# Optimization experiments

Hardware: AMD Instinct MI355X
Metric: run time of the kernel (lower is better)

## Reference

```python
import jax, jax.numpy as jnp
import numpy as np

N, E = 20000, 320000
H = 4            # heads per layer
C_IN, C_HID, C_OUT = 128, 64, 64
NEG_SLOPE = 0.2  # PyG GATConv default leaky_relu slope


def setup_inputs() -> dict:
    key = jax.random.key(0)
    ks = jax.random.split(key, 16)
    p = lambda k, shape: jax.random.normal(k, shape, jnp.float32) * 0.1
    return {
        "x": jax.random.normal(ks[0], (N, C_IN), jnp.float32),
        "edge_index": jax.random.randint(ks[1], (2, E), 0, N),
        # layer 0: in C_IN -> H*C_HID (concat)
        "W0": p(ks[2], (C_IN, H * C_HID)),
        "as0": p(ks[3], (H, C_HID)),
        "ad0": p(ks[4], (H, C_HID)),
        "b0": jnp.zeros((H * C_HID,), jnp.float32),
        # layer 1: in H*C_HID -> H*C_HID (concat)
        "W1": p(ks[5], (H * C_HID, H * C_HID)),
        "as1": p(ks[6], (H, C_HID)),
        "ad1": p(ks[7], (H, C_HID)),
        "b1": jnp.zeros((H * C_HID,), jnp.float32),
        # output layer: in H*C_HID -> C_OUT (mean over heads, concat=False)
        "W2": p(ks[8], (H * C_HID, H * C_OUT)),
        "as2": p(ks[9], (H, C_OUT)),
        "ad2": p(ks[10], (H, C_OUT)),
        "b2": jnp.zeros((C_OUT,), jnp.float32),
    }


def _gat_layer(x, src, dst, W, a_src, a_dst, b, concat):
    """PyG GATConv (eval mode): gather -> edge attention -> segment softmax -> scatter."""
    n = x.shape[0]
    h = (x @ W).reshape(n, H, -1)                      # [N, H, C]
    e_src = (h * a_src).sum(-1)                        # [N, H]
    e_dst = (h * a_dst).sum(-1)                        # [N, H]
    logits = jax.nn.leaky_relu(e_src[src] + e_dst[dst], NEG_SLOPE)   # [E', H]
    m = jax.lax.stop_gradient(jax.ops.segment_max(logits, dst, num_segments=n))
    ex = jnp.exp(logits - m[dst])
    denom = jax.ops.segment_sum(ex, dst, num_segments=n)
    alpha = ex / denom[dst]                            # [E', H] segment softmax per dst node
    out = jax.ops.segment_sum(h[src] * alpha[:, :, None], dst, num_segments=n)  # [N, H, C]
    out = out.reshape(n, -1) if concat else out.mean(axis=1)
    return out + b, alpha


def reference(x, edge_index, W0, as0, ad0, b0, W1, as1, ad1, b1, W2, as2, ad2, b2):
    n = x.shape[0]
    loops = jnp.arange(n, dtype=edge_index.dtype)      # GATConv adds self-loops
    src = jnp.concatenate([edge_index[0], loops])
    dst = jnp.concatenate([edge_index[1], loops])
    h, a0 = _gat_layer(x, src, dst, W0, as0, ad0, b0, True)
    h = jax.nn.elu(h)
    h, a1 = _gat_layer(h, src, dst, W1, as1, ad1, b1, True)
    h = jax.nn.elu(h)
    out, a2 = _gat_layer(h, src, dst, W2, as2, ad2, b2, False)
    return out, a0, a1, a2
```

## Files before the change

### kernel.cpp

```cpp
#include <hip/hip_runtime.h>
#include <hip/hip_bf16.h>
#include <math.h>

#define HCOLS 256
#define NHEAD 4
#define CDIM  64
#define NEG_SLOPE 0.2f

typedef __attribute__((ext_vector_type(8))) short bf16x8;
typedef __attribute__((ext_vector_type(4))) float f32x4;

__device__ __forceinline__ float leaky(float v) { return v > 0.f ? v : v * NEG_SLOPE; }
__device__ __forceinline__ unsigned short f2bf(float f) {
    unsigned u = __float_as_uint(f);
    u += 0x7fff + ((u >> 16) & 1);
    return (unsigned short)(u >> 16);
}
__device__ __forceinline__ float bf2f(unsigned short b) {
    return __uint_as_float(((unsigned)b) << 16);
}

__global__ void deg_kernel(const int* __restrict__ ei, int* __restrict__ deg,
                           int E, int Ep) {
    int e = blockIdx.x * 256 + threadIdx.x;
    if (e >= Ep) return;
    int d = (e < E) ? ei[E + e] : (e - E);
    atomicAdd(&deg[d], 1);
}

__global__ void scan_kernel(const int* __restrict__ deg, int* __restrict__ rowptr,
                            int* __restrict__ cursor, int n) {
    __shared__ int wsum[16];
    int tid = threadIdx.x;
    int lane = tid & 63, w = tid >> 6;
    int CH = (n + 1023) >> 10;
    int base = tid * CH;
    int s = 0;
    for (int k = 0; k < CH; ++k) {
        int i = base + k;
        s += (i < n) ? deg[i] : 0;
    }
    int incl = s;
#pragma unroll
    for (int d = 1; d < 64; d <<= 1) {
        int t = __shfl_up(incl, d, 64);
        if (lane >= d) incl += t;
    }
    if (lane == 63) wsum[w] = incl;
    __syncthreads();
    if (w == 0) {
        int v = (lane < 16) ? wsum[lane] : 0;
#pragma unroll
        for (int d = 1; d < 16; d <<= 1) {
            int t = __shfl_up(v, d, 64);
            if (lane >= d) v += t;
        }
        if (lane < 16) wsum[lane] = v;
    }
    __syncthreads();
    int woff = (w == 0) ? 0 : wsum[w - 1];
    int run = woff + incl - s;
    for (int k = 0; k < CH; ++k) {
        int i = base + k;
        if (i < n) { rowptr[i] = run; cursor[i] = run; run += deg[i]; }
    }
    if (tid == 1023) rowptr[n] = run;
}

__global__ void fill_kernel(const int* __restrict__ ei, int* __restrict__ cursor,
                            int* __restrict__ eidx, int E, int Ep) {
    int e = blockIdx.x * 256 + threadIdx.x;
    if (e >= Ep) return;
    int d = (e < E) ? ei[E + e] : (e - E);
    int pos = atomicAdd(&cursor[d], 1);
    eidx[pos] = e;
}

__global__ void wconv_kernel(const float* __restrict__ W, unsigned short* __restrict__ Wt, int K) {
    __shared__ float t[32][33];
    int bx = blockIdx.x;
    int by = blockIdx.y;
    int tx = threadIdx.x & 31, ty = threadIdx.x >> 5;
#pragma unroll
    for (int i = 0; i < 32; i += 8)
        t[ty + i][tx] = W[(by * 32 + ty + i) * HCOLS + bx * 32 + tx];
    __syncthreads();
#pragma unroll
    for (int i = 0; i < 32; i += 8)
        Wt[(size_t)(bx * 32 + ty + i) * K + by * 32 + tx] = f2bf(t[tx][ty + i]);
}

template <int K, bool SRC_F32>
__global__ void gemm_kernel(const void* __restrict__ Xv, const unsigned short* __restrict__ Wt,
                            unsigned short* __restrict__ Hout,
                            const float* __restrict__ As, const float* __restrict__ Ad,
                            float* __restrict__ esrc, float* __restrict__ edst,
                            int n) {
    constexpr int LDK = K + 16;
    __shared__ __align__(16) unsigned short a_sh[32 * LDK];
    int row0 = blockIdx.x * 32;
    int tid = threadIdx.x;

    constexpr int CH = 32 * K / 8;
    for (int c = tid; c < CH; c += 256) {
        int r = c / (K / 8), kc = c % (K / 8);
        int row = row0 + r;
        uint4 pack;
        if (row < n) {
            if (SRC_F32) {
                const float* X = (const float*)Xv;
                float4 f0 = *reinterpret_cast<const float4*>(&X[(size_t)row * K + kc * 8]);
                float4 f1 = *reinterpret_cast<const float4*>(&X[(size_t)row * K + kc * 8 + 4]);
                pack.x = f2bf(f0.x) | ((unsigned)f2bf(f0.y) << 16);
                pack.y = f2bf(f0.z) | ((unsigned)f2bf(f0.w) << 16);
                pack.z = f2bf(f1.x) | ((unsigned)f2bf(f1.y) << 16);
                pack.w = f2bf(f1.z) | ((unsigned)f2bf(f1.w) << 16);
            } else {
                const uint4* X = (const uint4*)Xv;
                pack = X[((size_t)row * K + kc * 8) / 8];
            }
        } else {
            pack = make_uint4(0, 0, 0, 0);
        }
        *reinterpret_cast<uint4*>(&a_sh[r * LDK + kc * 8]) = pack;
    }
    __syncthreads();

    int lane = tid & 63;
    int w = tid >> 6;
    int lr = lane & 15;
    int lk = (lane >> 4) * 8;

    f32x4 acc[2][4];
#pragma unroll
    for (int m = 0; m < 2; ++m)
#pragma unroll
        for (int nf = 0; nf < 4; ++nf) acc[m][nf] = (f32x4){0.f, 0.f, 0.f, 0.f};

    const unsigned short* wt = Wt + (size_t)(w * 64) * K;
#pragma unroll
    for (int ks = 0; ks < K / 32; ++ks) {
        bf16x8 a[2], b[4];
#pragma unroll
        for (int m = 0; m < 2; ++m)
            a[m] = *reinterpret_cast<const bf16x8*>(&a_sh[(16 * m + lr) * LDK + ks * 32 + lk]);
#pragma unroll
        for (int nf = 0; nf < 4; ++nf)
            b[nf] = *reinterpret_cast<const bf16x8*>(&wt[(size_t)(16 * nf + lr) * K + ks * 32 + lk]);
#pragma unroll
        for (int m = 0; m < 2; ++m)
#pragma unroll
            for (int nf = 0; nf < 4; ++nf)
                acc[m][nf] = __builtin_amdgcn_mfma_f32_16x16x32_bf16(a[m], b[nf], acc[m][nf], 0, 0, 0);
    }

    float as_v[4], ad_v[4];
#pragma unroll
    for (int nf = 0; nf < 4; ++nf) {
        as_v[nf] = As[w * 64 + 16 * nf + lr];
        ad_v[nf] = Ad[w * 64 + 16 * nf + lr];
    }
#pragma unroll
    for (int m = 0; m < 2; ++m) {
#pragma unroll
        for (int j = 0; j < 4; ++j) {
            int row_g = row0 + 16 * m + (lane >> 4) * 4 + j;
            bool ok = row_g < n;
#pragma unroll
            for (int nf = 0; nf < 4; ++nf) {
                if (ok) Hout[(size_t)row_g * HCOLS + w * 64 + 16 * nf + lr] = f2bf(acc[m][nf][j]);
            }
            float ps = acc[m][0][j] * as_v[0] + acc[m][1][j] * as_v[1] +
                       acc[m][2][j] * as_v[2] + acc[m][3][j] * as_v[3];
            float pd = acc[m][0][j] * ad_v[0] + acc[m][1][j] * ad_v[1] +
                       acc[m][2][j] * ad_v[2] + acc[m][3][j] * ad_v[3];
#pragma unroll
            for (int off = 1; off < 16; off <<= 1) {
                ps += __shfl_xor(ps, off, 64);
                pd += __shfl_xor(pd, off, 64);
            }
            if (lr == 0 && ok) {
                esrc[row_g * NHEAD + w] = ps;
                edst[row_g * NHEAD + w] = pd;
            }
        }
    }
}

template <int MODE>
__global__ void attn_agg_kernel(const unsigned short* __restrict__ h,
                                const float* __restrict__ esrc,
                                const float* __restrict__ edst,
                                const int* __restrict__ ei,
                                const int* __restrict__ rowptr,
                                const int* __restrict__ eidx,
                                const float* __restrict__ bias,
                                float* __restrict__ alpha,
                                void* __restrict__ xout,
                                int n, int E) {
    __shared__ __align__(16) float aT[4][NHEAD][72];
    __shared__ __align__(16) int   sArr[4][64];

    int wave = threadIdx.x >> 6;
    int lane = threadIdx.x & 63;
    int node = blockIdx.x * 4 + wave;
    if (node >= n) return;
    int s0 = rowptr[node], s1 = rowptr[node + 1];
    int deg = s1 - s0;
    float4 ed = *reinterpret_cast<const float4*>(&edst[node * NHEAD]);

    int i0 = s0 + lane;
    bool valid = i0 < s1;
    int e0 = 0, sv = 0;
    float4 lg0 = make_float4(-3.4e38f, -3.4e38f, -3.4e38f, -3.4e38f);
    if (valid) {
        e0 = eidx[i0];
        sv = (e0 < E) ? ei[e0] : (e0 - E);
        float4 es = *reinterpret_cast<const float4*>(&esrc[sv * NHEAD]);
        lg0.x = leaky(es.x + ed.x);
        lg0.y = leaky(es.y + ed.y);
        lg0.z = leaky(es.z + ed.z);
        lg0.w = leaky(es.w + ed.w);
    }
    float4 mx = lg0;
    for (int i = i0 + 64; i < s1; i += 64) {
        int e = eidx[i];
        int s = (e < E) ? ei[e] : (e - E);
        float4 es = *reinterpret_cast<const float4*>(&esrc[s * NHEAD]);
        mx.x = fmaxf(mx.x, leaky(es.x + ed.x));
        mx.y = fmaxf(mx.y, leaky(es.y + ed.y));
        mx.z = fmaxf(mx.z, leaky(es.z + ed.z));
        mx.w = fmaxf(mx.w, leaky(es.w + ed.w));
    }
#pragma unroll
    for (int off = 32; off; off >>= 1) {
        mx.x = fmaxf(mx.x, __shfl_xor(mx.x, off, 64));
        mx.y = fmaxf(mx.y, __shfl_xor(mx.y, off, 64));
        mx.z = fmaxf(mx.z, __shfl_xor(mx.z, off, 64));
        mx.w = fmaxf(mx.w, __shfl_xor(mx.w, off, 64));
    }
    float4 ex0 = make_float4(0.f, 0.f, 0.f, 0.f);
    if (valid) {
        ex0.x = __expf(lg0.x - mx.x);
        ex0.y = __expf(lg0.y - mx.y);
        ex0.z = __expf(lg0.z - mx.z);
        ex0.w = __expf(lg0.w - mx.w);
    }
    float4 sm = ex0;
    for (int i = i0 + 64; i < s1; i += 64) {
        int e = eidx[i];
        int s = (e < E) ? ei[e] : (e - E);
        float4 es = *reinterpret_cast<const float4*>(&esrc[s * NHEAD]);
        sm.x += __expf(leaky(es.x + ed.x) - mx.x);
        sm.y += __expf(leaky(es.y + ed.y) - mx.y);
        sm.z += __expf(leaky(es.z + ed.z) - mx.z);
        sm.w += __expf(leaky(es.w + ed.w) - mx.w);
    }
#pragma unroll
    for (int off = 32; off; off >>= 1) {
        sm.x += __shfl_xor(sm.x, off, 64);
        sm.y += __shfl_xor(sm.y, off, 64);
        sm.z += __shfl_xor(sm.z, off, 64);
        sm.w += __shfl_xor(sm.w, off, 64);
    }
    float4 inv = make_float4(1.f / sm.x, 1.f / sm.y, 1.f / sm.z, 1.f / sm.w);
    float4 al = make_float4(ex0.x * inv.x, ex0.y * inv.y, ex0.z * inv.z, ex0.w * inv.w);
    if (valid) *reinterpret_cast<float4*>(&alpha[(size_t)e0 * NHEAD]) = al;
    for (int i = i0 + 64; i < s1; i += 64) {
        int e = eidx[i];
        int s = (e < E) ? ei[e] : (e - E);
        float4 es = *reinterpret_cast<const float4*>(&esrc[s * NHEAD]);
        float4 av;
        av.x = __expf(leaky(es.x + ed.x) - mx.x) * inv.x;
        av.y = __expf(leaky(es.y + ed.y) - mx.y) * inv.y;
        av.z = __expf(leaky(es.z + ed.z) - mx.z) * inv.z;
        av.w = __expf(leaky(es.w + ed.w) - mx.w) * inv.w;
        *reinterpret_cast<float4*>(&alpha[(size_t)e * NHEAD]) = av;
    }
    bool big = deg > 64;
    if (big) __threadfence();

    aT[wave][0][lane] = valid ? al.x : 0.f;
    aT[wave][1][lane] = valid ? al.y : 0.f;
    aT[wave][2][lane] = valid ? al.z : 0.f;
    aT[wave][3][lane] = valid ? al.w : 0.f;
    sArr[wave][lane] = valid ? sv : 0;
    asm volatile("s_waitcnt lgkmcnt(0)" ::: "memory");
    __builtin_amdgcn_sched_barrier(0);

    int head = lane >> 4;
    unsigned laneoff = (unsigned)(lane << 3);
    const char* hb = (const char*)h;
    float4 acc = make_float4(0.f, 0.f, 0.f, 0.f);
    int m = deg < 64 ? deg : 64;
    int m4 = (m + 3) & ~3;
    const float* aTp = &aT[wave][head][0];
    const int*   sp  = &sArr[wave][0];
    for (int j = 0; j < m4; j += 4) {
        float4 a4 = *reinterpret_cast<const float4*>(aTp + j);
        int4   s4 = *reinterpret_cast<const int4*>(sp + j);
        uint2 h0 = *reinterpret_cast<const uint2*>(hb + (((unsigned)s4.x << 9) + laneoff));
        uint2 h1 = *reinterpret_cast<const uint2*>(hb + (((unsigned)s4.y << 9) + laneoff));
        uint2 h2 = *reinterpret_cast<const uint2*>(hb + (((unsigned)s4.z << 9) + laneoff));
        uint2 h3 = *reinterpret_cast<const uint2*>(hb + (((unsigned)s4.w << 9) + laneoff));
        acc.x = fmaf(a4.x, bf2f((unsigned short)(h0.x & 0xffff)), acc.x);
        acc.y = fmaf(a4.x, bf2f((unsigned short)(h0.x >> 16)),    acc.y);
        acc.z = fmaf(a4.x, bf2f((unsigned short)(h0.y & 0xffff)), acc.z);
        acc.w = fmaf(a4.x, bf2f((unsigned short)(h0.y >> 16)),    acc.w);
        acc.x = fmaf(a4.y, bf2f((unsigned short)(h1.x & 0xffff)), acc.x);
        acc.y = fmaf(a4.y, bf2f((unsigned short)(h1.x >> 16)),    acc.y);
        acc.z = fmaf(a4.y, bf2f((unsigned short)(h1.y & 0xffff)), acc.z);
        acc.w = fmaf(a4.y, bf2f((unsigned short)(h1.y >> 16)),    acc.w);
        acc.x = fmaf(a4.z, bf2f((unsigned short)(h2.x & 0xffff)), acc.x);
        acc.y = fmaf(a4.z, bf2f((unsigned short)(h2.x >> 16)),    acc.y);
        acc.z = fmaf(a4.z, bf2f((unsigned short)(h2.y & 0xffff)), acc.z);
        acc.w = fmaf(a4.z, bf2f((unsigned short)(h2.y >> 16)),    acc.w);
        acc.x = fmaf(a4.w, bf2f((unsigned short)(h3.x & 0xffff)), acc.x);
        acc.y = fmaf(a4.w, bf2f((unsigned short)(h3.x >> 16)),    acc.y);
        acc.z = fmaf(a4.w, bf2f((unsigned short)(h3.y & 0xffff)), acc.z);
        acc.w = fmaf(a4.w, bf2f((unsigned short)(h3.y >> 16)),    acc.w);
    }
    if (big) {
        for (int i = s0 + 64; i < s1; ++i) {
            int e = eidx[i];
            int s = (e < E) ? ei[e] : (e - E);
            float4 av = *reinterpret_cast<const float4*>(&alpha[(size_t)e * NHEAD]);
            float a = (head & 2) ? ((head & 1) ? av.w : av.z) : ((head & 1) ? av.y : av.x);
            uint2 hv = *reinterpret_cast<const uint2*>(hb + (((unsigned)s << 9) + laneoff));
            acc.x = fmaf(a, bf2f((unsigned short)(hv.x & 0xffff)), acc.x);
            acc.y = fmaf(a, bf2f((unsigned short)(hv.x >> 16)),    acc.y);
            acc.z = fmaf(a, bf2f((unsigned short)(hv.y & 0xffff)), acc.z);
            acc.w = fmaf(a, bf2f((unsigned short)(hv.y >> 16)),    acc.w);
        }
    }
    if (MODE == 0) {
        float4 bv = *reinterpret_cast<const float4*>(&bias[lane << 2]);
        float4 v;
        v.x = acc.x + bv.x; v.y = acc.y + bv.y; v.z = acc.z + bv.z; v.w = acc.w + bv.w;
        v.x = v.x > 0.f ? v.x : expm1f(v.x);
        v.y = v.y > 0.f ? v.y : expm1f(v.y);
        v.z = v.z > 0.f ? v.z : expm1f(v.z);
        v.w = v.w > 0.f ? v.w : expm1f(v.w);
        ushort4 o;
        o.x = f2bf(v.x); o.y = f2bf(v.y); o.z = f2bf(v.z); o.w = f2bf(v.w);
        *reinterpret_cast<ushort4*>(&((unsigned short*)xout)[(size_t)node * HCOLS + (lane << 2)]) = o;
    } else {
        acc.x += __shfl_xor(acc.x, 16, 64); acc.x += __shfl_xor(acc.x, 32, 64);
        acc.y += __shfl_xor(acc.y, 16, 64); acc.y += __shfl_xor(acc.y, 32, 64);
        acc.z += __shfl_xor(acc.z, 16, 64); acc.z += __shfl_xor(acc.z, 32, 64);
        acc.w += __shfl_xor(acc.w, 16, 64); acc.w += __shfl_xor(acc.w, 32, 64);
        if (lane < 16) {
            float4 bv = *reinterpret_cast<const float4*>(&bias[lane << 2]);
            float4 v;
            v.x = acc.x * 0.25f + bv.x;
            v.y = acc.y * 0.25f + bv.y;
            v.z = acc.z * 0.25f + bv.z;
            v.w = acc.w * 0.25f + bv.w;
            *reinterpret_cast<float4*>(&((float*)xout)[(size_t)node * CDIM + (lane << 2)]) = v;
        }
    }
}

extern "C" void kernel_launch(void* const* d_in, const int* in_sizes, int n_in,
                              void* d_out, int out_size, void* d_ws, size_t ws_size,
                              hipStream_t stream) {
    const float* x   = (const float*)d_in[0];
    const int*   ei  = (const int*)d_in[1];
    const float* W0  = (const float*)d_in[2];
    const float* as0 = (const float*)d_in[3];
    const float* ad0 = (const float*)d_in[4];
    const float* b0  = (const float*)d_in[5];
    const float* W1  = (const float*)d_in[6];
    const float* as1 = (const float*)d_in[7];
    const float* ad1 = (const float*)d_in[8];
    const float* b1  = (const float*)d_in[9];
    const float* W2  = (const float*)d_in[10];
    const float* as2 = (const float*)d_in[11];
    const float* ad2 = (const float*)d_in[12];
    const float* b2  = (const float*)d_in[13];

    const int N  = in_sizes[0] / 128;
    const int E  = in_sizes[1] / 2;
    const int Ep = E + N;

    float* out = (float*)d_out;
    float* a0  = out + (size_t)N * CDIM;
    float* a1  = a0 + (size_t)Ep * NHEAD;
    float* a2  = a1 + (size_t)Ep * NHEAD;

    char* wp = (char*)d_ws;
    auto carve = [&](size_t bytes) {
        char* p = wp;
        wp += (bytes + 255) & ~(size_t)255;
        return (void*)p;
    };
    unsigned short* hbuf = (unsigned short*)carve((size_t)N * HCOLS * 2);
    unsigned short* xbuf = (unsigned short*)carve((size_t)N * HCOLS * 2);
    float* esrc   = (float*)carve((size_t)N * NHEAD * 4);
    float* edst   = (float*)carve((size_t)N * NHEAD * 4);
    int*   deg    = (int*)carve((size_t)N * 4);
    int*   rowptr = (int*)carve((size_t)(N + 1) * 4);
    int*   cursor = (int*)carve((size_t)N * 4);
    int*   eidx   = (int*)carve((size_t)Ep * 4);
    unsigned short* Wt0 = (unsigned short*)carve((size_t)HCOLS * 128 * 2);
    unsigned short* Wt1 = (unsigned short*)carve((size_t)HCOLS * HCOLS * 2);
    unsigned short* Wt2 = (unsigned short*)carve((size_t)HCOLS * HCOLS * 2);

    hipMemsetAsync(deg, 0, (size_t)N * 4, stream);
    deg_kernel<<<(Ep + 255) / 256, 256, 0, stream>>>(ei, deg, E, Ep);
    scan_kernel<<<1, 1024, 0, stream>>>(deg, rowptr, cursor, N);
    fill_kernel<<<(Ep + 255) / 256, 256, 0, stream>>>(ei, cursor, eidx, E, Ep);

    wconv_kernel<<<dim3(8, 4), 256, 0, stream>>>(W0, Wt0, 128);
    wconv_kernel<<<dim3(8, 8), 256, 0, stream>>>(W1, Wt1, 256);
    wconv_kernel<<<dim3(8, 8), 256, 0, stream>>>(W2, Wt2, 256);

    int gemm_grid = (N + 31) / 32;
    int agg_grid  = (N + 3) / 4;

    gemm_kernel<128, true><<<gemm_grid, 256, 0, stream>>>(x, Wt0, hbuf, as0, ad0, esrc, edst, N);
    attn_agg_kernel<0><<<agg_grid, 256, 0, stream>>>(hbuf, esrc, edst, ei, rowptr, eidx, b0, a0, xbuf, N, E);

    gemm_kernel<256, false><<<gemm_grid, 256, 0, stream>>>(xbuf, Wt1, hbuf, as1, ad1, esrc, edst, N);
    attn_agg_kernel<0><<<agg_grid, 256, 0, stream>>>(hbuf, esrc, edst, ei, rowptr, eidx, b1, a1, xbuf, N, E);

    gemm_kernel<256, false><<<gemm_grid, 256, 0, stream>>>(xbuf, Wt2, hbuf, as2, ad2, esrc, edst, N);
    attn_agg_kernel<1><<<agg_grid, 256, 0, stream>>>(hbuf, esrc, edst, ei, rowptr, eidx, b2, a2, out, N, E);
}
```

Before: 244.1 us.

## Process 16 nodes per block with 16-lane softmax groups and 16-byte gathers

Restructures the attention-aggregation kernel so each 16-lane group computes the softmax for one destination node, letting one wave cover four nodes. The wave then aggregates those four nodes one after another, using 16-byte bf16 loads split across two half-waves. This targets the wasted lanes when average degree (~17) is far below 64, and it halves the number of gather instructions. Other changes: the memset becomes a small kernel, and the three weight conversions merge into one launch. The trade-offs are more register pressure, a serial per-node loop inside each wave, and a single-lane-group path for nodes with degree above 64.

```diff
diff --git a/kernel.cpp b/kernel.cpp
--- a/kernel.cpp
+++ b/kernel.cpp
@@ -16,8 +16,21 @@
     u += 0x7fff + ((u >> 16) & 1);
     return (unsigned short)(u >> 16);
 }
-__device__ __forceinline__ float bf2f(unsigned short b) {
-    return __uint_as_float(((unsigned)b) << 16);
+
+__device__ __forceinline__ void fma8(float* acc, uint4 hv, float a) {
+    acc[0] = fmaf(a, __uint_as_float(hv.x << 16),          acc[0]);
+    acc[1] = fmaf(a, __uint_as_float(hv.x & 0xffff0000u),  acc[1]);
+    acc[2] = fmaf(a, __uint_as_float(hv.y << 16),          acc[2]);
+    acc[3] = fmaf(a, __uint_as_float(hv.y & 0xffff0000u),  acc[3]);
+    acc[4] = fmaf(a, __uint_as_float(hv.z << 16),          acc[4]);
+    acc[5] = fmaf(a, __uint_as_float(hv.z & 0xffff0000u),  acc[5]);
+    acc[6] = fmaf(a, __uint_as_float(hv.w << 16),          acc[6]);
+    acc[7] = fmaf(a, __uint_as_float(hv.w & 0xffff0000u),  acc[7]);
+}
+
+__global__ void zero_deg_kernel(int* __restrict__ deg, int n) {
+    int i = blockIdx.x * 256 + threadIdx.x;
+    if (i < n) deg[i] = 0;
 }
 
 __global__ void deg_kernel(const int* __restrict__ ei, int* __restrict__ deg,
@@ -76,8 +89,16 @@
     eidx[pos] = e;
 }
 
-__global__ void wconv_kernel(const float* __restrict__ W, unsigned short* __restrict__ Wt, int K) {
+__global__ void wconv_kernel(const float* __restrict__ W0, const float* __restrict__ W1,
+                             const float* __restrict__ W2,
+                             unsigned short* __restrict__ Wt0, unsigned short* __restrict__ Wt1,
+                             unsigned short* __restrict__ Wt2) {
     __shared__ float t[32][33];
+    int z = blockIdx.z;
+    const float* W = (z == 0) ? W0 : (z == 1) ? W1 : W2;
+    unsigned short* Wt = (z == 0) ? Wt0 : (z == 1) ? Wt1 : Wt2;
+    int K = (z == 0) ? 128 : 256;
+    if (blockIdx.y * 32 >= K) return;
     int bx = blockIdx.x;
     int by = blockIdx.y;
     int tx = threadIdx.x & 31, ty = threadIdx.x >> 5;
@@ -188,6 +209,7 @@
 }
 
 template <int MODE>
+__launch_bounds__(256, 4)
 __global__ void attn_agg_kernel(const unsigned short* __restrict__ h,
                                 const float* __restrict__ esrc,
                                 const float* __restrict__ edst,
@@ -198,32 +220,51 @@
                                 float* __restrict__ alpha,
                                 void* __restrict__ xout,
                                 int n, int E) {
-    __shared__ __align__(16) float aT[4][NHEAD][72];
-    __shared__ __align__(16) int   sArr[4][64];
-
-    int wave = threadIdx.x >> 6;
-    int lane = threadIdx.x & 63;
-    int node = blockIdx.x * 4 + wave;
-    if (node >= n) return;
-    int s0 = rowptr[node], s1 = rowptr[node + 1];
+    __shared__ __align__(16) float aT[16][64][NHEAD];
+    __shared__ int sArr[16][64];
+
+    int tid = threadIdx.x;
+    int wave = tid >> 6, lane = tid & 63;
+    int g = lane >> 4, t = lane & 15;
+    int nodeblk = blockIdx.x * 16;
+    int nidx = wave * 4 + g;
+    int node = nodeblk + nidx;
+    bool gvalid = node < n;
+    int s0 = 0, s1 = 0;
+    if (gvalid) { s0 = rowptr[node]; s1 = rowptr[node + 1]; }
     int deg = s1 - s0;
-    float4 ed = *reinterpret_cast<const float4*>(&edst[node * NHEAD]);
-
-    int i0 = s0 + lane;
-    bool valid = i0 < s1;
-    int e0 = 0, sv = 0;
-    float4 lg0 = make_float4(-3.4e38f, -3.4e38f, -3.4e38f, -3.4e38f);
-    if (valid) {
-        e0 = eidx[i0];
-        sv = (e0 < E) ? ei[e0] : (e0 - E);
-        float4 es = *reinterpret_cast<const float4*>(&esrc[sv * NHEAD]);
-        lg0.x = leaky(es.x + ed.x);
-        lg0.y = leaky(es.y + ed.y);
-        lg0.z = leaky(es.z + ed.z);
-        lg0.w = leaky(es.w + ed.w);
-    }
-    float4 mx = lg0;
-    for (int i = i0 + 64; i < s1; i += 64) {
+    float4 ed = make_float4(0.f, 0.f, 0.f, 0.f);
+    if (gvalid) ed = *reinterpret_cast<const float4*>(&edst[node * NHEAD]);
+
+    const float NEGINF = -3.4e38f;
+    float4 lgc[4]; int sc[4], ec[4];
+    int degc = deg < 64 ? deg : 64;
+    int nch = (degc + 15) >> 4;
+    float4 mx = make_float4(NEGINF, NEGINF, NEGINF, NEGINF);
+#pragma unroll
+    for (int c = 0; c < 4; ++c) {
+        sc[c] = 0; ec[c] = 0;
+        lgc[c] = make_float4(NEGINF, NEGINF, NEGINF, NEGINF);
+        if (c < nch) {
+            int i = s0 + c * 16 + t;
+            bool v = i < s1;
+            int e = v ? eidx[i] : 0;
+            int s = v ? ((e < E) ? ei[e] : (e - E)) : 0;
+            sc[c] = s; ec[c] = e;
+            if (v) {
+                float4 es = *reinterpret_cast<const float4*>(&esrc[s * NHEAD]);
+                lgc[c].x = leaky(es.x + ed.x);
+                lgc[c].y = leaky(es.y + ed.y);
+                lgc[c].z = leaky(es.z + ed.z);
+                lgc[c].w = leaky(es.w + ed.w);
+            }
+            mx.x = fmaxf(mx.x, lgc[c].x);
+            mx.y = fmaxf(mx.y, lgc[c].y);
+            mx.z = fmaxf(mx.z, lgc[c].z);
+            mx.w = fmaxf(mx.w, lgc[c].w);
+        }
+    }
+    for (int i = s0 + 64 + t; i < s1; i += 16) {
         int e = eidx[i];
         int s = (e < E) ? ei[e] : (e - E);
         float4 es = *reinterpret_cast<const float4*>(&esrc[s * NHEAD]);
@@ -233,21 +274,26 @@
         mx.w = fmaxf(mx.w, leaky(es.w + ed.w));
     }
 #pragma unroll
-    for (int off = 32; off; off >>= 1) {
+    for (int off = 1; off < 16; off <<= 1) {
         mx.x = fmaxf(mx.x, __shfl_xor(mx.x, off, 64));
         mx.y = fmaxf(mx.y, __shfl_xor(mx.y, off, 64));
         mx.z = fmaxf(mx.z, __shfl_xor(mx.z, off, 64));
         mx.w = fmaxf(mx.w, __shfl_xor(mx.w, off, 64));
     }
-    float4 ex0 = make_float4(0.f, 0.f, 0.f, 0.f);
-    if (valid) {
-        ex0.x = __expf(lg0.x - mx.x);
-        ex0.y = __expf(lg0.y - mx.y);
-        ex0.z = __expf(lg0.z - mx.z);
-        ex0.w = __expf(lg0.w - mx.w);
-    }
-    float4 sm = ex0;
-    for (int i = i0 + 64; i < s1; i += 64) {
+    float4 exc[4];
+    float4 sm = make_float4(0.f, 0.f, 0.f, 0.f);
+#pragma unroll
+    for (int c = 0; c < 4; ++c) {
+        exc[c] = make_float4(0.f, 0.f, 0.f, 0.f);
+        if (c < nch) {
+            exc[c].x = __expf(lgc[c].x - mx.x);
+            exc[c].y = __expf(lgc[c].y - mx.y);
+            exc[c].z = __expf(lgc[c].z - mx.z);
+            exc[c].w = __expf(lgc[c].w - mx.w);
+            sm.x += exc[c].x; sm.y += exc[c].y; sm.z += exc[c].z; sm.w += exc[c].w;
+        }
+    }
+    for (int i = s0 + 64 + t; i < s1; i += 16) {
         int e = eidx[i];
         int s = (e < E) ? ei[e] : (e - E);
         float4 es = *reinterpret_cast<const float4*>(&esrc[s * NHEAD]);
@@ -257,16 +303,26 @@
         sm.w += __expf(leaky(es.w + ed.w) - mx.w);
     }
 #pragma unroll
-    for (int off = 32; off; off >>= 1) {
+    for (int off = 1; off < 16; off <<= 1) {
         sm.x += __shfl_xor(sm.x, off, 64);
         sm.y += __shfl_xor(sm.y, off, 64);
         sm.z += __shfl_xor(sm.z, off, 64);
         sm.w += __shfl_xor(sm.w, off, 64);
     }
     float4 inv = make_float4(1.f / sm.x, 1.f / sm.y, 1.f / sm.z, 1.f / sm.w);
-    float4 al = make_float4(ex0.x * inv.x, ex0.y * inv.y, ex0.z * inv.z, ex0.w * inv.w);
-    if (valid) *reinterpret_cast<float4*>(&alpha[(size_t)e0 * NHEAD]) = al;
-    for (int i = i0 + 64; i < s1; i += 64) {
+#pragma unroll
+    for (int c = 0; c < 4; ++c) {
+        if (c < nch) {
+            float4 al4;
+            al4.x = exc[c].x * inv.x; al4.y = exc[c].y * inv.y;
+            al4.z = exc[c].z * inv.z; al4.w = exc[c].w * inv.w;
+            int i = s0 + c * 16 + t;
+            if (i < s1) *reinterpret_cast<float4*>(&alpha[(size_t)ec[c] * NHEAD]) = al4;
+            *reinterpret_cast<float4*>(&aT[nidx][c * 16 + t][0]) = al4;
+            sArr[nidx][c * 16 + t] = sc[c];
+        }
+    }
+    for (int i = s0 + 64 + t; i < s1; i += 16) {
         int e = eidx[i];
         int s = (e < E) ? ei[e] : (e - E);
         float4 es = *reinterpret_cast<const float4*>(&esrc[s * NHEAD]);
@@ -277,86 +333,101 @@
         av.w = __expf(leaky(es.w + ed.w) - mx.w) * inv.w;
         *reinterpret_cast<float4*>(&alpha[(size_t)e * NHEAD]) = av;
     }
-    bool big = deg > 64;
-    if (big) __threadfence();
-
-    aT[wave][0][lane] = valid ? al.x : 0.f;
-    aT[wave][1][lane] = valid ? al.y : 0.f;
-    aT[wave][2][lane] = valid ? al.z : 0.f;
-    aT[wave][3][lane] = valid ? al.w : 0.f;
-    sArr[wave][lane] = valid ? sv : 0;
+    if (__any(deg > 64)) __threadfence();
+
     asm volatile("s_waitcnt lgkmcnt(0)" ::: "memory");
     __builtin_amdgcn_sched_barrier(0);
 
-    int head = lane >> 4;
-    unsigned laneoff = (unsigned)(lane << 3);
+    int half = lane >> 5;
+    int q = lane & 31;
+    int head = q >> 3;
+    unsigned byteoff = (unsigned)q * 16u;
     const char* hb = (const char*)h;
-    float4 acc = make_float4(0.f, 0.f, 0.f, 0.f);
-    int m = deg < 64 ? deg : 64;
-    int m4 = (m + 3) & ~3;
-    const float* aTp = &aT[wave][head][0];
-    const int*   sp  = &sArr[wave][0];
-    for (int j = 0; j < m4; j += 4) {
-        float4 a4 = *reinterpret_cast<const float4*>(aTp + j);
-        int4   s4 = *reinterpret_cast<const int4*>(sp + j);
-        uint2 h0 = *reinterpret_cast<const uint2*>(hb + (((unsigned)s4.x << 9) + laneoff));
-        uint2 h1 = *reinterpret_cast<const uint2*>(hb + (((unsigned)s4.y << 9) + laneoff));
-        uint2 h2 = *reinterpret_cast<const uint2*>(hb + (((unsigned)s4.z << 9) + laneoff));
-        uint2 h3 = *reinterpret_cast<const uint2*>(hb + (((unsigned)s4.w << 9) + laneoff));
-        acc.x = fmaf(a4.x, bf2f((unsigned short)(h0.x & 0xffff)), acc.x);
-        acc.y = fmaf(a4.x, bf2f((unsigned short)(h0.x >> 16)),    acc.y);
-        acc.z = fmaf(a4.x, bf2f((unsigned short)(h0.y & 0xffff)), acc.z);
-        acc.w = fmaf(a4.x, bf2f((unsigned short)(h0.y >> 16)),    acc.w);
-        acc.x = fmaf(a4.y, bf2f((unsigned short)(h1.x & 0xffff)), acc.x);
-        acc.y = fmaf(a4.y, bf2f((unsigned short)(h1.x >> 16)),    acc.y);
-        acc.z = fmaf(a4.y, bf2f((unsigned short)(h1.y & 0xffff)), acc.z);
-        acc.w = fmaf(a4.y, bf2f((unsigned short)(h1.y >> 16)),    acc.w);
-        acc.x = fmaf(a4.z, bf2f((unsigned short)(h2.x & 0xffff)), acc.x);
-        acc.y = fmaf(a4.z, bf2f((unsigned short)(h2.x >> 16)),    acc.y);
-        acc.z = fmaf(a4.z, bf2f((unsigned short)(h2.y & 0xffff)), acc.z);
-        acc.w = fmaf(a4.z, bf2f((unsigned short)(h2.y >> 16)),    acc.w);
-        acc.x = fmaf(a4.w, bf2f((unsigned short)(h3.x & 0xffff)), acc.x);
-        acc.y = fmaf(a4.w, bf2f((unsigned short)(h3.x >> 16)),    acc.y);
-        acc.z = fmaf(a4.w, bf2f((unsigned short)(h3.y & 0xffff)), acc.z);
-        acc.w = fmaf(a4.w, bf2f((unsigned short)(h3.y >> 16)),    acc.w);
-    }
-    if (big) {
-        for (int i = s0 + 64; i < s1; ++i) {
-            int e = eidx[i];
-            int s = (e < E) ? ei[e] : (e - E);
-            float4 av = *reinterpret_cast<const float4*>(&alpha[(size_t)e * NHEAD]);
-            float a = (head & 2) ? ((head & 1) ? av.w : av.z) : ((head & 1) ? av.y : av.x);
-            uint2 hv = *reinterpret_cast<const uint2*>(hb + (((unsigned)s << 9) + laneoff));
-            acc.x = fmaf(a, bf2f((unsigned short)(hv.x & 0xffff)), acc.x);
-            acc.y = fmaf(a, bf2f((unsigned short)(hv.x >> 16)),    acc.y);
-            acc.z = fmaf(a, bf2f((unsigned short)(hv.y & 0xffff)), acc.z);
-            acc.w = fmaf(a, bf2f((unsigned short)(hv.y >> 16)),    acc.w);
-        }
-    }
-    if (MODE == 0) {
-        float4 bv = *reinterpret_cast<const float4*>(&bias[lane << 2]);
-        float4 v;
-        v.x = acc.x + bv.x; v.y = acc.y + bv.y; v.z = acc.z + bv.z; v.w = acc.w + bv.w;
-        v.x = v.x > 0.f ? v.x : expm1f(v.x);
-        v.y = v.y > 0.f ? v.y : expm1f(v.y);
-        v.z = v.z > 0.f ? v.z : expm1f(v.z);
-        v.w = v.w > 0.f ? v.w : expm1f(v.w);
-        ushort4 o;
-        o.x = f2bf(v.x); o.y = f2bf(v.y); o.z = f2bf(v.z); o.w = f2bf(v.w);
-        *reinterpret_cast<ushort4*>(&((unsigned short*)xout)[(size_t)node * HCOLS + (lane << 2)]) = o;
-    } else {
-        acc.x += __shfl_xor(acc.x, 16, 64); acc.x += __shfl_xor(acc.x, 32, 64);
-        acc.y += __shfl_xor(acc.y, 16, 64); acc.y += __shfl_xor(acc.y, 32, 64);
-        acc.z += __shfl_xor(acc.z, 16, 64); acc.z += __shfl_xor(acc.z, 32, 64);
-        acc.w += __shfl_xor(acc.w, 16, 64); acc.w += __shfl_xor(acc.w, 32, 64);
-        if (lane < 16) {
-            float4 bv = *reinterpret_cast<const float4*>(&bias[lane << 2]);
-            float4 v;
-            v.x = acc.x * 0.25f + bv.x;
-            v.y = acc.y * 0.25f + bv.y;
-            v.z = acc.z * 0.25f + bv.z;
-            v.w = acc.w * 0.25f + bv.w;
-            *reinterpret_cast<float4*>(&((float*)xout)[(size_t)node * CDIM + (lane << 2)]) = v;
+
+    for (int g2 = 0; g2 < 4; ++g2) {
+        int nd = nodeblk + wave * 4 + g2;
+        if (nd >= n) break;
+        int t0 = rowptr[nd], t1 = rowptr[nd + 1];
+        int dg = t1 - t0;
+        int m = dg < 64 ? dg : 64;
+        int m2 = (m + 1) & ~1;
+        const float* ap = &aT[wave * 4 + g2][0][0] + head;
+        const int* sp = &sArr[wave * 4 + g2][0];
+        float acc[8];
+#pragma unroll
+        for (int k = 0; k < 8; ++k) acc[k] = 0.f;
+        int j = 0;
+        for (; j + 4 <= m2; j += 4) {
+            int jA = j + half, jB = j + 2 + half;
+            int sA = sp[jA], sB = sp[jB];
+            float aA = ap[jA * NHEAD], aB = ap[jB * NHEAD];
+            uint4 hA = *reinterpret_cast<const uint4*>(hb + (((unsigned)sA) << 9) + byteoff);
+            uint4 hB = *reinterpret_cast<const uint4*>(hb + (((unsigned)sB) << 9) + byteoff);
+            fma8(acc, hA, aA);
+            fma8(acc, hB, aB);
+        }
+        for (; j < m2; j += 2) {
+            int jA = j + half;
+            int sA = sp[jA];
+            float aA = ap[jA * NHEAD];
+            uint4 hA = *reinterpret_cast<const uint4*>(hb + (((unsigned)sA) << 9) + byteoff);
+            fma8(acc, hA, aA);
+        }
+        if (dg > 64) {
+            for (int i = t0 + 64; i < t1; ++i) {
+                if (half == 0) {
+                    int e = eidx[i];
+                    int s = (e < E) ? ei[e] : (e - E);
+                    float a = alpha[(size_t)e * NHEAD + head];
+                    uint4 hv = *reinterpret_cast<const uint4*>(hb + (((unsigned)s) << 9) + byteoff);
+                    fma8(acc, hv, a);
+                }
+            }
+        }
+#pragma unroll
+        for (int k = 0; k < 8; ++k) acc[k] += __shfl_xor(acc[k], 32, 64);
+
+        if (MODE == 0) {
+            if (half == 0) {
+                float4 b0 = *reinterpret_cast<const float4*>(&bias[q * 8]);
+                float4 b1 = *reinterpret_cast<const float4*>(&bias[q * 8 + 4]);
+                float v0 = acc[0] + b0.x, v1 = acc[1] + b0.y, v2 = acc[2] + b0.z, v3 = acc[3] + b0.w;
+                float v4 = acc[4] + b1.x, v5 = acc[5] + b1.y, v6 = acc[6] + b1.z, v7 = acc[7] + b1.w;
+                v0 = v0 > 0.f ? v0 : expm1f(v0);
+                v1 = v1 > 0.f ? v1 : expm1f(v1);
+                v2 = v2 > 0.f ? v2 : expm1f(v2);
+                v3 = v3 > 0.f ? v3 : expm1f(v3);
+                v4 = v4 > 0.f ? v4 : expm1f(v4);
+                v5 = v5 > 0.f ? v5 : expm1f(v5);
+                v6 = v6 > 0.f ? v6 : expm1f(v6);
+                v7 = v7 > 0.f ? v7 : expm1f(v7);
+                uint4 o;
+                o.x = (unsigned)f2bf(v0) | ((unsigned)f2bf(v1) << 16);
+                o.y = (unsigned)f2bf(v2) | ((unsigned)f2bf(v3) << 16);
+                o.z = (unsigned)f2bf(v4) | ((unsigned)f2bf(v5) << 16);
+                o.w = (unsigned)f2bf(v6) | ((unsigned)f2bf(v7) << 16);
+                *reinterpret_cast<uint4*>(&((unsigned short*)xout)[(size_t)nd * HCOLS + q * 8]) = o;
+            }
+        } else {
+#pragma unroll
+            for (int k = 0; k < 8; ++k) {
+                acc[k] += __shfl_xor(acc[k], 8, 64);
+                acc[k] += __shfl_xor(acc[k], 16, 64);
+            }
+            if (half == 0 && q < 8) {
+                float* op = (float*)xout + (size_t)nd * CDIM + q * 8;
+                float4 r0, r1;
+                r0.x = acc[0] * 0.25f + bias[q * 8 + 0];
+                r0.y = acc[1] * 0.25f + bias[q * 8 + 1];
+                r0.z = acc[2] * 0.25f + bias[q * 8 + 2];
+                r0.w = acc[3] * 0.25f + bias[q * 8 + 3];
+                r1.x = acc[4] * 0.25f + bias[q * 8 + 4];
+                r1.y = acc[5] * 0.25f + bias[q * 8 + 5];
+                r1.z = acc[6] * 0.25f + bias[q * 8 + 6];
+                r1.w = acc[7] * 0.25f + bias[q * 8 + 7];
+                *reinterpret_cast<float4*>(op) = r0;
+                *reinterpret_cast<float4*>(op + 4) = r1;
+            }
         }
     }
 }
@@ -406,17 +477,15 @@
     unsigned short* Wt1 = (unsigned short*)carve((size_t)HCOLS * HCOLS * 2);
     unsigned short* Wt2 = (unsigned short*)carve((size_t)HCOLS * HCOLS * 2);
 
-    hipMemsetAsync(deg, 0, (size_t)N * 4, stream);
+    zero_deg_kernel<<<(N + 255) / 256, 256, 0, stream>>>(deg, N);
     deg_kernel<<<(Ep + 255) / 256, 256, 0, stream>>>(ei, deg, E, Ep);
     scan_kernel<<<1, 1024, 0, stream>>>(deg, rowptr, cursor, N);
     fill_kernel<<<(Ep + 255) / 256, 256, 0, stream>>>(ei, cursor, eidx, E, Ep);
 
-    wconv_kernel<<<dim3(8, 4), 256, 0, stream>>>(W0, Wt0, 128);
-    wconv_kernel<<<dim3(8, 8), 256, 0, stream>>>(W1, Wt1, 256);
-    wconv_kernel<<<dim3(8, 8), 256, 0, stream>>>(W2, Wt2, 256);
+    wconv_kernel<<<dim3(8, 8, 3), 256, 0, stream>>>(W0, W1, W2, Wt0, Wt1, Wt2);
 
     int gemm_grid = (N + 31) / 32;
-    int agg_grid  = (N + 3) / 4;
+    int agg_grid  = (N + 15) / 16;
 
     gemm_kernel<128, true><<<gemm_grid, 256, 0, stream>>>(x, Wt0, hbuf, as0, ad0, esrc, edst, N);
     attn_agg_kernel<0><<<agg_grid, 256, 0, stream>>>(hbuf, esrc, edst, ei, rowptr, eidx, b0, a0, xbuf, N, E);
```

New measurement: 233.5 us. 1.05x faster.
